# Kernel tuning notes

Hardware: AMD Instinct MI355X
Metric: run time of the kernel (lower is better)

## Reference

```python
import jax, jax.numpy as jnp
import numpy as np

EMBED_DIM = 1024
NUM_HEADS = 16
HEAD_DIM = EMBED_DIM // NUM_HEADS
SCALE = 1.0 / np.sqrt(HEAD_DIM).astype(np.float32)


def setup_inputs() -> dict:
    key = jax.random.key(0)
    ks = jax.random.split(key, 9)
    B, T, C = 2, 2048, EMBED_DIM
    s = 1.0 / np.sqrt(C).astype(np.float32)  # torch Linear init scale (approx, uniform bound)
    return {
        "x_q": jax.random.normal(ks[0], (B, T, C), dtype=jnp.float32),
        "attn_mask": jnp.zeros((T, T), dtype=jnp.float32),
        "Wq": jax.random.uniform(ks[1], (C, C), jnp.float32, -s, s),
        "bq": jax.random.uniform(ks[2], (C,), jnp.float32, -s, s),
        "Wk": jax.random.uniform(ks[3], (C, C), jnp.float32, -s, s),
        "bk": jax.random.uniform(ks[4], (C,), jnp.float32, -s, s),
        "Wv": jax.random.uniform(ks[5], (C, C), jnp.float32, -s, s),
        "bv": jax.random.uniform(ks[6], (C,), jnp.float32, -s, s),
        "Wo": jax.random.uniform(ks[7], (C, C), jnp.float32, -s, s),
        "bo": jax.random.uniform(ks[8], (C,), jnp.float32, -s, s),
    }


def reference(x_q, attn_mask, Wq, bq, Wk, bk, Wv, bv, Wo, bo):
    B, Tq, C = x_q.shape
    # self-attention: x_kv = x_q
    q = (x_q @ Wq.T + bq).reshape(B, Tq, NUM_HEADS, HEAD_DIM)
    k = (x_q @ Wk.T + bk).reshape(B, Tq, NUM_HEADS, HEAD_DIM)
    v = (x_q @ Wv.T + bv).reshape(B, Tq, NUM_HEADS, HEAD_DIM)
    # (B, H, Tq, Tk)
    scores = jnp.einsum('bqhd,bkhd->bhqk', q, k) * SCALE
    scores = scores + attn_mask[None, None, :, :]  # 2D additive mask path
    attn = jax.nn.softmax(scores, axis=-1)  # dropout p=0.0 -> identity
    out = jnp.einsum('bhqk,bkhd->bqhd', attn, v).reshape(B, Tq, C)
    out = out @ Wo.T + bo
    return out
```

## Files before the change

### kernel.cpp

```cpp
#include <hip/hip_runtime.h>
#include <hip/hip_bf16.h>
#include <stdint.h>

typedef _Float16 f16x8_t __attribute__((ext_vector_type(8)));
typedef _Float16 f16x4_t __attribute__((ext_vector_type(4)));
typedef float    f32x4_t __attribute__((ext_vector_type(4)));
typedef float    f32x16_t __attribute__((ext_vector_type(16)));

#define T_SEQ 2048
#define NH    16
#define HD    64
#define CDIM  1024
#define NTOK  4096
#define QSCALE 0.18033688011112042f
#define LOG2E  1.4426950408889634f

__device__ __forceinline__ void async_ld16(void* lds, const void* g) {
    __builtin_amdgcn_global_load_lds(
        (const __attribute__((address_space(1))) uint32_t*)g,
        (__attribute__((address_space(3))) uint32_t*)lds, 16, 0, 0);
}

__global__ __launch_bounds__(256)
void prep_all(const float* __restrict__ x, const float* __restrict__ Wq,
              const float* __restrict__ Wk, const float* __restrict__ Wv,
              const float* __restrict__ Wo, const float* __restrict__ mask,
              _Float16* __restrict__ xh, _Float16* __restrict__ Wqkvh,
              _Float16* __restrict__ Woh, int* __restrict__ flag)
{
    const int XQ = NTOK * CDIM / 4;
    const int WQ = CDIM * CDIM / 4;
    int i = blockIdx.x * 256 + threadIdx.x;
    if (i < XQ + 4 * WQ) {
        const float* s; _Float16* d; int off;
        if (i < XQ) { s = x; d = xh; off = i; }
        else {
            int j = i - XQ; int w = j >> 18; off = j & (WQ - 1);
            s = (w == 0) ? Wq : (w == 1) ? Wk : (w == 2) ? Wv : Wo;
            d = (w == 3) ? Woh : Wqkvh + (size_t)w * CDIM * CDIM;
        }
        float4 v = ((const float4*)s)[off];
        f16x4_t h = {(_Float16)v.x, (_Float16)v.y, (_Float16)v.z, (_Float16)v.w};
        ((f16x4_t*)d)[off] = h;
    } else {
        int off = i - (XQ + 4 * WQ);
        float4 v = ((const float4*)mask)[off];
        if (v.x != 0.f || v.y != 0.f || v.z != 0.f || v.w != 0.f) atomicOr(flag, 1);
    }
}

template<int MODE>
__global__ __launch_bounds__(256)
void gemm_f16(const _Float16* __restrict__ Ag, const _Float16* __restrict__ Bg,
              const float* __restrict__ b0, const float* __restrict__ b1,
              const float* __restrict__ b2,
              _Float16* __restrict__ Qo, _Float16* __restrict__ Ko,
              _Float16* __restrict__ Vto, float* __restrict__ Fo)
{
    __shared__ _Float16 sA[2][128 * 32];
    __shared__ _Float16 sB[2][128 * 32];
    const int K = CDIM;
    const int NBX = (MODE == 0) ? 24 : 8;
    const int NWG = NBX * 32;
    const int tid  = threadIdx.x;
    const int lane = tid & 63, wv = tid >> 6;
    const int wr = wv >> 1, wc = wv & 1;
    const int bid = blockIdx.x;
    const int swz = (bid & 7) * (NWG / 8) + (bid >> 3);
    const int rowA0 = (swz % NBX) * 128;
    const int rowB0 = (swz / NBX) * 128;
    const int srow = lane >> 2;
    const int scol = (lane & 3) * 8;
    const int fr = lane & 15, fg = lane >> 4;
    f32x4_t acc[4][4] = {};

#define STAGE(buf, kk) do {                                                     \
        _Pragma("unroll")                                                       \
        for (int i_ = 0; i_ < 2; ++i_) {                                        \
            const int eoff = i_ * 2048 + wv * 512;                              \
            const int r_ = i_ * 64 + wv * 16 + srow;                            \
            async_ld16(&sA[buf][eoff], Ag + (size_t)(rowA0 + r_) * K + (kk) + scol); \
            async_ld16(&sB[buf][eoff], Bg + (size_t)(rowB0 + r_) * K + (kk) + scol); \
        } } while (0)

    STAGE(0, 0);
    for (int k0 = 0; k0 < K; k0 += 32) {
        const int cur = (k0 >> 5) & 1;
        __syncthreads();
        if (k0 + 32 < K) STAGE(cur ^ 1, k0 + 32);
        f16x8_t a[4], b[4];
#pragma unroll
        for (int mi = 0; mi < 4; ++mi)
            a[mi] = *(const f16x8_t*)&sA[cur][(wr * 64 + mi * 16 + fr) * 32 + fg * 8];
#pragma unroll
        for (int ni = 0; ni < 4; ++ni)
            b[ni] = *(const f16x8_t*)&sB[cur][(wc * 64 + ni * 16 + fr) * 32 + fg * 8];
#pragma unroll
        for (int mi = 0; mi < 4; ++mi)
#pragma unroll
            for (int ni = 0; ni < 4; ++ni)
                acc[mi][ni] = __builtin_amdgcn_mfma_f32_16x16x32_f16(a[mi], b[ni], acc[mi][ni], 0, 0, 0);
    }
#undef STAGE

    if (MODE == 0) {
        const int which = rowA0 >> 10;
        const float* bp = (which == 0) ? b0 : ((which == 1) ? b1 : b2);
#pragma unroll
        for (int mi = 0; mi < 4; ++mi) {
            const int cc = (rowA0 & 1023) + wr * 64 + mi * 16 + fg * 4;
            const float4 bv = *(const float4*)&bp[cc];
            const int h = cc >> 6, d0 = cc & 63;
#pragma unroll
            for (int ni = 0; ni < 4; ++ni) {
                const int tok = rowB0 + wc * 64 + ni * 16 + fr;
                const int bh = (tok >> 11) * NH + h, tt = tok & (T_SEQ - 1);
                const float v0 = acc[mi][ni][0] + bv.x, v1 = acc[mi][ni][1] + bv.y;
                const float v2 = acc[mi][ni][2] + bv.z, v3 = acc[mi][ni][3] + bv.w;
                if (which == 0) {
                    f16x4_t hq = {(_Float16)(v0 * QSCALE), (_Float16)(v1 * QSCALE),
                                  (_Float16)(v2 * QSCALE), (_Float16)(v3 * QSCALE)};
                    *(f16x4_t*)&Qo[((size_t)bh * T_SEQ + tt) * HD + d0] = hq;
                } else if (which == 1) {
                    f16x4_t hk = {(_Float16)v0, (_Float16)v1, (_Float16)v2, (_Float16)v3};
                    *(f16x4_t*)&Ko[((size_t)bh * 32 + (tt >> 6)) * 4096 +
                                   (d0 >> 3) * 512 + (tt & 63) * 8 + (d0 & 7)] = hk;
                } else {
                    const size_t vb_ = ((size_t)bh * 32 + (tt >> 6)) * 4096 +
                                       (size_t)((tt >> 3) & 7) * 512 + (tt & 7);
                    Vto[vb_ + (d0 + 0) * 8] = (_Float16)v0;
                    Vto[vb_ + (d0 + 1) * 8] = (_Float16)v1;
                    Vto[vb_ + (d0 + 2) * 8] = (_Float16)v2;
                    Vto[vb_ + (d0 + 3) * 8] = (_Float16)v3;
                }
            }
        }
    } else {
#pragma unroll
        for (int mi = 0; mi < 4; ++mi) {
            const int cc = rowA0 + wr * 64 + mi * 16 + fg * 4;
            const float4 bv = *(const float4*)&b0[cc];
#pragma unroll
            for (int ni = 0; ni < 4; ++ni) {
                const int tok = rowB0 + wc * 64 + ni * 16 + fr;
                float4 ov = {acc[mi][ni][0] + bv.x, acc[mi][ni][1] + bv.y,
                             acc[mi][ni][2] + bv.z, acc[mi][ni][3] + bv.w};
                *(float4*)&Fo[(size_t)tok * CDIM + cc] = ov;
            }
        }
    }
}

__global__ __launch_bounds__(256, 2)
void attn_f16(const _Float16* __restrict__ Q, const _Float16* __restrict__ Kc,
              const _Float16* __restrict__ Vc, const float* __restrict__ mask,
              const int* __restrict__ mflag, _Float16* __restrict__ AO)
{
    __shared__ __align__(16) _Float16 sK[2][4096];
    __shared__ __align__(16) _Float16 sV[2][4096];

    const int tid = threadIdx.x;
    const int lane = tid & 63, wv = tid >> 6;
    const int ln = lane & 31, hi = lane >> 5;
    const int bid = blockIdx.x;
    const int swz = (bid & 7) * 64 + (bid >> 3);
    const int qx = swz & 15, bh = swz >> 4;
    const int b = bh >> 4, h = bh & (NH - 1);
    const int q0 = qx * 128 + wv * 32;
    const _Float16* Qb  = Q  + (size_t)bh * T_SEQ * HD;
    const _Float16* Kbh = Kc + (size_t)bh * (T_SEQ * HD);
    const _Float16* Vbh = Vc + (size_t)bh * (T_SEQ * HD);
    const int soff = tid * 8;

    f16x8_t qf[4];
#pragma unroll
    for (int dc = 0; dc < 4; ++dc)
        qf[dc] = *(const f16x8_t*)&Qb[(size_t)(q0 + ln) * HD + dc * 16 + hi * 8];

    f32x16_t o0 = {}, o1 = {};
    float m_run = -1e30f, l_run = 0.f;
    const int mf = mflag[0];

    async_ld16(&sK[0][soff],        Kbh + soff);
    async_ld16(&sK[0][2048 + soff], Kbh + 2048 + soff);
    async_ld16(&sV[0][soff],        Vbh + soff);
    async_ld16(&sV[0][2048 + soff], Vbh + 2048 + soff);

    for (int t = 0; t < T_SEQ / 64; ++t) {
        const int cur = t & 1;
        __syncthreads();
        if (t + 1 < T_SEQ / 64) {
            const int nb = cur ^ 1, goff = (t + 1) * 4096;
            async_ld16(&sK[nb][soff],        Kbh + goff + soff);
            async_ld16(&sK[nb][2048 + soff], Kbh + goff + 2048 + soff);
            async_ld16(&sV[nb][soff],        Vbh + goff + soff);
            async_ld16(&sV[nb][2048 + soff], Vbh + goff + 2048 + soff);
        }

        f32x16_t s0 = {}, s1 = {};
        __builtin_amdgcn_s_setprio(1);
#pragma unroll
        for (int dc = 0; dc < 4; ++dc) {
            f16x8_t kf0 = *(const f16x8_t*)&sK[cur][(2 * dc + hi) * 512 + ln * 8];
            f16x8_t kf1 = *(const f16x8_t*)&sK[cur][(2 * dc + hi) * 512 + (32 + ln) * 8];
            s0 = __builtin_amdgcn_mfma_f32_32x32x16_f16(kf0, qf[dc], s0, 0, 0, 0);
            s1 = __builtin_amdgcn_mfma_f32_32x32x16_f16(kf1, qf[dc], s1, 0, 0, 0);
        }
        __builtin_amdgcn_s_setprio(0);

        if (mf) {
            const float* mrow = mask + (size_t)(q0 + ln) * T_SEQ + t * 64;
#pragma unroll
            for (int r2 = 0; r2 < 16; ++r2) {
                const int row = (r2 & 3) + 8 * (r2 >> 2) + 4 * hi;
                s0[r2] += mrow[row] * LOG2E;
                s1[r2] += mrow[32 + row] * LOG2E;
            }
        }

        float mt[8];
#pragma unroll
        for (int i = 0; i < 8; ++i)
            mt[i] = fmaxf(fmaxf(s0[2 * i], s0[2 * i + 1]), fmaxf(s1[2 * i], s1[2 * i + 1]));
#pragma unroll
        for (int st = 4; st > 0; st >>= 1)
#pragma unroll
            for (int i = 0; i < st; ++i) mt[i] = fmaxf(mt[i], mt[i + st]);
        float tmax = fmaxf(mt[0], __shfl_xor(mt[0], 32, 64));

        if (!__all(tmax <= m_run + 8.0f)) {
            const float mnew = fmaxf(m_run, tmax);
            const float sc = __builtin_amdgcn_exp2f(m_run - mnew);
            m_run = mnew;
            l_run *= sc;
#pragma unroll
            for (int r2 = 0; r2 < 16; ++r2) {
                const int row = (r2 & 3) + 8 * (r2 >> 2) + 4 * hi;
                const float scr = __shfl(sc, row, 64);
                o0[r2] *= scr;
                o1[r2] *= scr;
            }
        }

#pragma unroll
        for (int r2 = 0; r2 < 16; ++r2) {
            s0[r2] = __builtin_amdgcn_exp2f(s0[r2] - m_run);
            s1[r2] = __builtin_amdgcn_exp2f(s1[r2] - m_run);
        }
        float sm[8];
#pragma unroll
        for (int i = 0; i < 8; ++i)
            sm[i] = (s0[2 * i] + s0[2 * i + 1]) + (s1[2 * i] + s1[2 * i + 1]);
#pragma unroll
        for (int st = 4; st > 0; st >>= 1)
#pragma unroll
            for (int i = 0; i < st; ++i) sm[i] += sm[i + st];
        l_run += sm[0] + __shfl_xor(sm[0], 32, 64);

        f16x8_t pa[4];
#pragma unroll
        for (int g = 0; g < 2; ++g) {
            const f32x16_t& sg = g ? s1 : s0;
            uint32_t W[8];
#pragma unroll
            for (int t2 = 0; t2 < 8; ++t2) {
                auto pk = __builtin_amdgcn_cvt_pkrtz(sg[2 * t2], sg[2 * t2 + 1]);
                W[t2] = __builtin_bit_cast(uint32_t, pk);
            }
#pragma unroll
            for (int c2 = 0; c2 < 2; ++c2) {
                uint32_t a0 = W[4 * c2 + 0], a1 = W[4 * c2 + 1];
                uint32_t a2 = W[4 * c2 + 2], a3 = W[4 * c2 + 3];
                asm("v_permlane32_swap_b32 %0, %1" : "+v"(a0), "+v"(a2));
                asm("v_permlane32_swap_b32 %0, %1" : "+v"(a1), "+v"(a3));
                union { uint32_t w[4]; f16x8_t v; } u;
                u.w[0] = a0; u.w[1] = a1; u.w[2] = a2; u.w[3] = a3;
                pa[g * 2 + c2] = u.v;
            }
        }

        __builtin_amdgcn_s_setprio(1);
#pragma unroll
        for (int c = 0; c < 4; ++c) {
            f16x8_t vb0 = *(const f16x8_t*)&sV[cur][(2 * c + hi) * 512 + ln * 8];
            f16x8_t vb1 = *(const f16x8_t*)&sV[cur][(2 * c + hi) * 512 + (32 + ln) * 8];
            o0 = __builtin_amdgcn_mfma_f32_32x32x16_f16(pa[c], vb0, o0, 0, 0, 0);
            o1 = __builtin_amdgcn_mfma_f32_32x32x16_f16(pa[c], vb1, o1, 0, 0, 0);
        }
        __builtin_amdgcn_s_setprio(0);
    }

    const float linv = 1.f / l_run;
#pragma unroll
    for (int r2 = 0; r2 < 16; ++r2) {
        const int row = (r2 & 3) + 8 * (r2 >> 2) + 4 * hi;
        const float inv = __shfl(linv, row, 64);
        const size_t base = (size_t)(b * T_SEQ + q0 + row) * CDIM + h * HD;
        AO[base + ln]      = (_Float16)(o0[r2] * inv);
        AO[base + 32 + ln] = (_Float16)(o1[r2] * inv);
    }
}

extern "C" void kernel_launch(void* const* d_in, const int* in_sizes, int n_in,
                              void* d_out, int out_size, void* d_ws, size_t ws_size,
                              hipStream_t stream) {
    const float* x    = (const float*)d_in[0];
    const float* mask = (const float*)d_in[1];
    const float* Wq   = (const float*)d_in[2];
    const float* bq   = (const float*)d_in[3];
    const float* Wk   = (const float*)d_in[4];
    const float* bk   = (const float*)d_in[5];
    const float* Wv   = (const float*)d_in[6];
    const float* bv   = (const float*)d_in[7];
    const float* Wo   = (const float*)d_in[8];
    const float* bo   = (const float*)d_in[9];
    float* out = (float*)d_out;

    char* ws = (char*)d_ws;
    _Float16* xh    = (_Float16*)(ws);
    _Float16* Wqkvh = (_Float16*)(ws + (8u  << 20));
    _Float16* Woh   = (_Float16*)(ws + (14u << 20));
    _Float16* Qp    = (_Float16*)(ws + (16u << 20));
    _Float16* Kc    = (_Float16*)(ws + (24u << 20));
    _Float16* Vc    = (_Float16*)(ws + (32u << 20));
    int* mflag      = (int*)(ws + (40u << 20));
    _Float16* AO    = xh;

    hipMemsetAsync(mflag, 0, 4, stream);
    prep_all<<<12288, 256, 0, stream>>>(x, Wq, Wk, Wv, Wo, mask, xh, Wqkvh, Woh, mflag);
    gemm_f16<0><<<768, 256, 0, stream>>>(Wqkvh, xh, bq, bk, bv, Qp, Kc, Vc, nullptr);
    attn_f16<<<512, 256, 0, stream>>>(Qp, Kc, Vc, mask, mflag, AO);
    gemm_f16<1><<<256, 256, 0, stream>>>(Woh, AO, bo, nullptr, nullptr,
                                         nullptr, nullptr, nullptr, out);
}
```

Baseline: 131.0 us.

## Triple-buffer LDS stages with partial vmcnt waits and remap blocks per XCD

```diff
diff --git a/kernel.cpp b/kernel.cpp
--- a/kernel.cpp
+++ b/kernel.cpp
@@ -57,18 +57,17 @@
               _Float16* __restrict__ Qo, _Float16* __restrict__ Ko,
               _Float16* __restrict__ Vto, float* __restrict__ Fo)
 {
-    __shared__ _Float16 sA[2][128 * 32];
-    __shared__ _Float16 sB[2][128 * 32];
+    __shared__ _Float16 sA[3][128 * 32];
+    __shared__ _Float16 sB[3][128 * 32];
     const int K = CDIM;
-    const int NBX = (MODE == 0) ? 24 : 8;
-    const int NWG = NBX * 32;
     const int tid  = threadIdx.x;
     const int lane = tid & 63, wv = tid >> 6;
     const int wr = wv >> 1, wc = wv & 1;
     const int bid = blockIdx.x;
-    const int swz = (bid & 7) * (NWG / 8) + (bid >> 3);
-    const int rowA0 = (swz % NBX) * 128;
-    const int rowB0 = (swz / NBX) * 128;
+    const int xcd = bid & 7, L = bid >> 3;
+    const int sb = L & 31, st = L >> 5;
+    const int rowA0 = (st * 8 + (sb & 7)) * 128;
+    const int rowB0 = (xcd * 4 + (sb >> 3)) * 128;
     const int srow = lane >> 2;
     const int scol = (lane & 3) * 8;
     const int fr = lane & 15, fg = lane >> 4;
@@ -84,10 +83,17 @@
         } } while (0)
 
     STAGE(0, 0);
+    int cur = 0;
     for (int k0 = 0; k0 < K; k0 += 32) {
-        const int cur = (k0 >> 5) & 1;
-        __syncthreads();
-        if (k0 + 32 < K) STAGE(cur ^ 1, k0 + 32);
+        const int nxt = (cur == 2) ? 0 : cur + 1;
+        if (k0 + 32 < K) {
+            STAGE(nxt, k0 + 32);
+            asm volatile("s_waitcnt vmcnt(4)" ::: "memory");
+        } else {
+            asm volatile("s_waitcnt vmcnt(0)" ::: "memory");
+        }
+        __builtin_amdgcn_s_barrier();
+        __builtin_amdgcn_sched_barrier(0);
         f16x8_t a[4], b[4];
 #pragma unroll
         for (int mi = 0; mi < 4; ++mi)
@@ -100,6 +106,7 @@
 #pragma unroll
             for (int ni = 0; ni < 4; ++ni)
                 acc[mi][ni] = __builtin_amdgcn_mfma_f32_16x16x32_f16(a[mi], b[ni], acc[mi][ni], 0, 0, 0);
+        cur = nxt;
     }
 #undef STAGE
 
@@ -156,15 +163,16 @@
               const _Float16* __restrict__ Vc, const float* __restrict__ mask,
               const int* __restrict__ mflag, _Float16* __restrict__ AO)
 {
-    __shared__ __align__(16) _Float16 sK[2][4096];
-    __shared__ __align__(16) _Float16 sV[2][4096];
+    __shared__ __align__(16) _Float16 sK[3][4096];
+    __shared__ __align__(16) _Float16 sV[3][4096];
 
     const int tid = threadIdx.x;
     const int lane = tid & 63, wv = tid >> 6;
     const int ln = lane & 31, hi = lane >> 5;
     const int bid = blockIdx.x;
-    const int swz = (bid & 7) * 64 + (bid >> 3);
-    const int qx = swz & 15, bh = swz >> 4;
+    const int xcd = bid & 7, idx = bid >> 3;
+    const int bh = xcd * 4 + (idx & 3);
+    const int qx = idx >> 2;
     const int b = bh >> 4, h = bh & (NH - 1);
     const int q0 = qx * 128 + wv * 32;
     const _Float16* Qb  = Q  + (size_t)bh * T_SEQ * HD;
@@ -185,17 +193,22 @@
     async_ld16(&sK[0][2048 + soff], Kbh + 2048 + soff);
     async_ld16(&sV[0][soff],        Vbh + soff);
     async_ld16(&sV[0][2048 + soff], Vbh + 2048 + soff);
+    int cur = 0;
 
     for (int t = 0; t < T_SEQ / 64; ++t) {
-        const int cur = t & 1;
-        __syncthreads();
+        const int nxt = (cur == 2) ? 0 : cur + 1;
         if (t + 1 < T_SEQ / 64) {
-            const int nb = cur ^ 1, goff = (t + 1) * 4096;
-            async_ld16(&sK[nb][soff],        Kbh + goff + soff);
-            async_ld16(&sK[nb][2048 + soff], Kbh + goff + 2048 + soff);
-            async_ld16(&sV[nb][soff],        Vbh + goff + soff);
-            async_ld16(&sV[nb][2048 + soff], Vbh + goff + 2048 + soff);
-        }
+            const int goff = (t + 1) * 4096;
+            async_ld16(&sK[nxt][soff],        Kbh + goff + soff);
+            async_ld16(&sK[nxt][2048 + soff], Kbh + goff + 2048 + soff);
+            async_ld16(&sV[nxt][soff],        Vbh + goff + soff);
+            async_ld16(&sV[nxt][2048 + soff], Vbh + goff + 2048 + soff);
+            asm volatile("s_waitcnt vmcnt(4)" ::: "memory");
+        } else {
+            asm volatile("s_waitcnt vmcnt(0)" ::: "memory");
+        }
+        __builtin_amdgcn_s_barrier();
+        __builtin_amdgcn_sched_barrier(0);
 
         f32x16_t s0 = {}, s1 = {};
         __builtin_amdgcn_s_setprio(1);
@@ -288,6 +301,7 @@
             o1 = __builtin_amdgcn_mfma_f32_32x32x16_f16(pa[c], vb1, o1, 0, 0, 0);
         }
         __builtin_amdgcn_s_setprio(0);
+        cur = nxt;
     }
 
     const float linv = 1.f / l_run;
```

After: 128.9 us. Within noise of the previous version (-1.6%).
